# Kernel tuning notes

Hardware: AMD Instinct MI355X
Metric: run time of the kernel (lower is better)

## Reference

```python
import jax, jax.numpy as jnp
import numpy as np

D_MODEL = 1024
NUM_HEADS = 16
WINDOW = 128
DEPTH = D_MODEL // NUM_HEADS


def setup_inputs() -> dict:
    key = jax.random.key(0)
    ks = jax.random.split(key, 9)
    B, S = 2, 2048
    scale = 1.0 / np.sqrt(D_MODEL)
    x = jax.random.normal(ks[0], (B, S, D_MODEL), dtype=jnp.float32)
    Wq = jax.random.normal(ks[1], (D_MODEL, D_MODEL), dtype=jnp.float32) * scale
    Wk = jax.random.normal(ks[2], (D_MODEL, D_MODEL), dtype=jnp.float32) * scale
    Wv = jax.random.normal(ks[3], (D_MODEL, D_MODEL), dtype=jnp.float32) * scale
    Wo = jax.random.normal(ks[4], (D_MODEL, D_MODEL), dtype=jnp.float32) * scale
    bq = jnp.zeros((D_MODEL,), jnp.float32)
    bk = jnp.zeros((D_MODEL,), jnp.float32)
    bv = jnp.zeros((D_MODEL,), jnp.float32)
    bo = jnp.zeros((D_MODEL,), jnp.float32)
    return {"x": x, "Wq": Wq, "bq": bq, "Wk": Wk, "bk": bk,
            "Wv": Wv, "bv": bv, "Wo": Wo, "bo": bo}


def _split_heads(t, B, S):
    # [B,S,D] -> [B,H,S,depth]
    return t.reshape(B, S, NUM_HEADS, DEPTH).transpose(0, 2, 1, 3)


def reference(x, Wq, bq, Wk, bk, Wv, bv, Wo, bo):
    B, S, _ = x.shape
    q = _split_heads(x @ Wq + bq, B, S)
    k = _split_heads(x @ Wk + bk, B, S)
    v = _split_heads(x @ Wv + bv, B, S)
    scores = jnp.einsum('bhqd,bhkd->bhqk', q, k) / jnp.sqrt(jnp.float32(DEPTH))
    idx = jnp.arange(S)
    # mask[i_row=j, i_col=i] per original: |i - j| <= window (symmetric)
    local = jnp.abs(idx[None, :] - idx[:, None]) <= WINDOW  # [S,S]
    scores = jnp.where(local[None, None], scores, jnp.float32(-1e9))
    attn = jax.nn.softmax(scores, axis=-1)
    out = jnp.einsum('bhqk,bhkd->bhqd', attn, v)
    concat = out.transpose(0, 2, 1, 3).reshape(B, S, D_MODEL)
    return concat @ Wo + bo
```

## Files before the change

### kernel.cpp

```cpp
#include <hip/hip_runtime.h>
#include <cstdint>
#include <cstddef>

typedef __attribute__((ext_vector_type(8))) short short8;
typedef __attribute__((ext_vector_type(4))) short short4v;
typedef __attribute__((ext_vector_type(4))) float f32x4;
typedef short8 bf16x8;

typedef __attribute__((address_space(1))) const unsigned GU;
typedef __attribute__((address_space(3))) unsigned LU;

__device__ __forceinline__ short f2bf(float f) {
  unsigned u = __builtin_bit_cast(unsigned, f);
  u += 0x7fffu + ((u >> 16) & 1u);
  return (short)(u >> 16);
}

__global__ __launch_bounds__(256) void k_prep(const float* __restrict__ x,
                                              const float* __restrict__ W0, const float* __restrict__ W1,
                                              const float* __restrict__ W2, const float* __restrict__ W3,
                                              short* __restrict__ xb, short* __restrict__ WT) {
  __shared__ short T[64 * 72];
  int bid = blockIdx.x;
  int tid = threadIdx.x;
  if (bid < 2048) {
    size_t i = ((size_t)bid * 256 + tid) * 8;
    f32x4 a = *(const f32x4*)(x + i);
    f32x4 b = *(const f32x4*)(x + i + 4);
    short8 o;
#pragma unroll
    for (int j = 0; j < 4; ++j) { o[j] = f2bf(a[j]); o[4 + j] = f2bf(b[j]); }
    *(short8*)(xb + i) = o;
    return;
  }
  bid -= 2048;
  int widx = bid >> 8;
  int t = bid & 255;
  int kr = (t >> 4) * 64, nc = (t & 15) * 64;
  const float* W = widx == 0 ? W0 : widx == 1 ? W1 : widx == 2 ? W2 : W3;
  short* out = WT + (size_t)widx * 1048576;
#pragma unroll
  for (int i = 0; i < 4; ++i) {
    int idx = tid + i * 256;
    int k = idx >> 4, n4 = (idx & 15) << 2;
    f32x4 v = *(const f32x4*)(W + (size_t)(kr + k) * 1024 + nc + n4);
#pragma unroll
    for (int j = 0; j < 4; ++j) T[(n4 + j) * 72 + k] = f2bf(v[j]);
  }
  __syncthreads();
#pragma unroll
  for (int i = 0; i < 2; ++i) {
    int idx = tid + i * 256;
    int n = idx >> 3, k8 = (idx & 7) << 3;
    *(short8*)(out + (size_t)(nc + n) * 1024 + kr + k8) = *(const short8*)&T[n * 72 + k8];
  }
}

__global__ __launch_bounds__(256) void k_tv(const short* __restrict__ v, short* __restrict__ vT) {
  __shared__ short T[64 * 72];
  int bid = blockIdx.x;
  int stile = bid & 31, h = (bid >> 5) & 15, b = bid >> 9;
  int s0 = stile * 64;
  int tid = threadIdx.x;
#pragma unroll
  for (int i = 0; i < 2; ++i) {
    int idx = tid + i * 256;
    int s = idx >> 3, d0 = (idx & 7) << 3;
    short8 vec = *(const short8*)(v + ((size_t)b * 2048 + s0 + s) * 1024 + h * 64 + d0);
#pragma unroll
    for (int j = 0; j < 8; ++j) T[(d0 + j) * 72 + s] = vec[j];
  }
  __syncthreads();
#pragma unroll
  for (int i = 0; i < 2; ++i) {
    int idx = tid + i * 256;
    int d = idx >> 3, s8 = (idx & 7) << 3;
    *(short8*)(vT + (((size_t)b * 16 + h) * 64 + d) * 2048 + s0 + s8) = *(const short8*)&T[d * 72 + s8];
  }
}

__global__ __launch_bounds__(512, 1) void k_gemm256(
    const short* __restrict__ A, const short* __restrict__ BT,
    const float* __restrict__ bias0, const float* __restrict__ bias1, const float* __restrict__ bias2,
    short* __restrict__ outb) {
  __shared__ short S[57344];
  const int tid = threadIdx.x;
  const int lane = tid & 63, w = tid >> 6;
  const int g = lane >> 4, qi = lane & 15;
  const int wm = w >> 2, wn = w & 3;
  int bid = blockIdx.x;
  int swz = (bid & 7) * 32 + (bid >> 3);
  const int tm = swz >> 4, tn = swz & 15;
  const int m0 = tm * 256, n0 = tn * 192;
  const size_t K = 1024;
  const short* Ab = A + (size_t)m0 * K;
  const short* Bb = BT + (size_t)n0 * K;

  auto stage64 = [&](int roff, const short* gbase, int kt) {
    int r = tid >> 3;
    int js = ((tid & 7) ^ (r & 7)) << 3;
    __builtin_amdgcn_global_load_lds((GU*)(gbase + (size_t)r * K + kt * 64 + js),
                                     (LU*)(&S[roff + tid * 8]), 16, 0, 0);
  };
  auto lda_a = [&](int bbase, int mf, int kk) -> bf16x8 {
    int row = (mf & 3) * 16 + qi;
    int reg = wm * 2 + (mf >> 2);
    return *(const bf16x8*)&S[bbase + reg * 4096 + row * 64 + (((kk * 4 + g) ^ (row & 7)) << 3)];
  };
  auto lda_b = [&](int bbase, int nf, int kk) -> bf16x8 {
    int c = wn * 48 + nf * 16 + qi;
    int reg = c >> 6, row = c & 63;
    return *(const bf16x8*)&S[bbase + 16384 + reg * 4096 + row * 64 + (((kk * 4 + g) ^ (row & 7)) << 3)];
  };

  f32x4 acc[8][3];
#pragma unroll
  for (int i = 0; i < 8; ++i)
#pragma unroll
    for (int j = 0; j < 3; ++j) acc[i][j] = (f32x4)(0.0f);

#define MFA(mi, ni, av, bv) \
  acc[mi][ni] = __builtin_amdgcn_mfma_f32_16x16x32_bf16(av, bv, acc[mi][ni], 0, 0, 0)
#define MF12(Aa, Bb_, o) \
  MFA((o)+0,0,(Aa)[(o)+0],(Bb_)[0]); MFA((o)+0,1,(Aa)[(o)+0],(Bb_)[1]); MFA((o)+0,2,(Aa)[(o)+0],(Bb_)[2]); \
  MFA((o)+1,0,(Aa)[(o)+1],(Bb_)[0]); MFA((o)+1,1,(Aa)[(o)+1],(Bb_)[1]); MFA((o)+1,2,(Aa)[(o)+1],(Bb_)[2]); \
  MFA((o)+2,0,(Aa)[(o)+2],(Bb_)[0]); MFA((o)+2,1,(Aa)[(o)+2],(Bb_)[1]); MFA((o)+2,2,(Aa)[(o)+2],(Bb_)[2]); \
  MFA((o)+3,0,(Aa)[(o)+3],(Bb_)[0]); MFA((o)+3,1,(Aa)[(o)+3],(Bb_)[1]); MFA((o)+3,2,(Aa)[(o)+3],(Bb_)[2])
#define SB __builtin_amdgcn_sched_barrier(0)
#define PHASE_TAIL(MFMAS) do { \
    SB; \
    __builtin_amdgcn_s_barrier(); \
    asm volatile("s_waitcnt lgkmcnt(0)" ::: "memory"); \
    SB; \
    __builtin_amdgcn_s_setprio(1); \
    MFMAS; \
    __builtin_amdgcn_s_setprio(0); \
    SB; \
    __builtin_amdgcn_s_barrier(); \
  } while (0)

  stage64(0,     Ab,            0);
  stage64(4096,  Ab + 65536,    0);
  stage64(8192,  Ab + 131072,   0);
  stage64(12288, Ab + 196608,   0);
  stage64(16384, Bb,            0);
  stage64(20480, Bb + 65536,    0);
  stage64(24576, Bb + 131072,   0);
  stage64(28672 + 16384, Bb,          1);
  stage64(28672 + 20480, Bb + 65536,  1);
  stage64(28672 + 24576, Bb + 131072, 1);
  asm volatile("s_waitcnt vmcnt(3)" ::: "memory");
  __builtin_amdgcn_s_barrier();

  for (int t = 0; t < 16; ++t) {
    const int b = t & 1, nb = b ^ 1;
    const int bb = b * 28672, nbb = nb * 28672;
    const int t1 = t + 1 < 15 ? t + 1 : 15;
    const int t2 = t + 2 < 15 ? t + 2 : 15;
    bf16x8 aA[8], aB[3], cA[8], cB[3];

#pragma unroll
    for (int mf = 0; mf < 4; ++mf) aA[mf] = lda_a(bb, mf, 0);
#pragma unroll
    for (int nf = 0; nf < 3; ++nf) aB[nf] = lda_b(bb, nf, 0);
    stage64(nbb,        Ab,         t1);
    stage64(nbb + 4096, Ab + 65536, t1);
    PHASE_TAIL(MF12(aA, aB, 0));
#pragma unroll
    for (int mf = 4; mf < 8; ++mf) aA[mf] = lda_a(bb, mf, 0);
#pragma unroll
    for (int nf = 0; nf < 3; ++nf) cB[nf] = lda_b(bb, nf, 1);
    stage64(nbb + 8192,  Ab + 131072, t1);
    stage64(nbb + 12288, Ab + 196608, t1);
    PHASE_TAIL(MF12(aA, aB, 4));
#pragma unroll
    for (int mf = 0; mf < 4; ++mf) cA[mf] = lda_a(bb, mf, 1);
    stage64(bb + 16384, Bb,         t2);
    stage64(bb + 20480, Bb + 65536, t2);
    PHASE_TAIL(MF12(cA, cB, 0));
#pragma unroll
    for (int mf = 4; mf < 8; ++mf) cA[mf] = lda_a(bb, mf, 1);
    stage64(bb + 24576, Bb + 131072, t2);
    asm volatile("s_waitcnt vmcnt(3)" ::: "memory");
    PHASE_TAIL(MF12(cA, cB, 4));
  }
#undef PHASE_TAIL
#undef MF12
#undef MFA
#undef SB

  asm volatile("s_waitcnt vmcnt(0)" ::: "memory");
  __syncthreads();
  float bv[3];
  int seln[3];
#pragma unroll
  for (int nf = 0; nf < 3; ++nf) {
    int colg = n0 + wn * 48 + nf * 16 + qi;
    int sel = colg >> 10;
    const float* bias = sel == 0 ? bias0 : (sel == 1 ? bias1 : bias2);
    bv[nf] = bias[colg & 1023];
    seln[nf] = sel;
    (void)seln;
  }
  short* Ep = S;
#pragma unroll
  for (int p = 0; p < 2; ++p) {
    __syncthreads();
    if (wm == p) {
#pragma unroll
      for (int mf = 0; mf < 8; ++mf)
#pragma unroll
        for (int nf = 0; nf < 3; ++nf)
#pragma unroll
          for (int j = 0; j < 4; ++j)
            Ep[(mf * 16 + g * 4 + j) * 200 + wn * 48 + nf * 16 + qi] =
                f2bf(acc[mf][nf][j] + bv[nf]);
    }
    __syncthreads();
#pragma unroll
    for (int i = 0; i < 6; ++i) {
      int idx = tid + i * 512;
      int r = idx / 24, c8 = (idx % 24) * 8;
      int grow = m0 + p * 128 + r;
      int colg = n0 + c8;
      int sel = colg >> 10;
      *(short8*)&outb[(size_t)sel * 4194304 + (size_t)grow * 1024 + (colg & 1023)] =
          *(const short8*)&Ep[r * 200 + c8];
    }
  }
}

__global__ __launch_bounds__(256, 2) void k_gemmO(
    const short* __restrict__ A, const short* __restrict__ BT,
    const float* __restrict__ bias0, float* __restrict__ outf) {
  __shared__ short Smem[16384];
  const int tid = threadIdx.x;
  const int lane = tid & 63, w = tid >> 6;
  const int g = lane >> 4, qi = lane & 15;
  const int wr = (w >> 1) * 64, wc = (w & 1) * 64;
  const int m0 = blockIdx.y * 128, n0 = blockIdx.x * 128;
  const size_t K = 1024;
  const short* Ab = A + (size_t)m0 * K;
  const short* Bb = BT + (size_t)n0 * K;

  auto stage = [&](int buf, int k0) {
    short* Asb = Smem + buf * 4096;
    short* Bsb = Smem + 8192 + buf * 4096;
#pragma unroll
    for (int i = 0; i < 2; ++i) {
      int cidx = tid + i * 256;
      int r = cidx >> 2;
      int csw = ((cidx & 3) ^ ((r >> 1) & 3)) << 3;
      __builtin_amdgcn_global_load_lds((GU*)(Ab + (size_t)r * K + k0 + csw),
                                       (LU*)(&Asb[cidx * 8]), 16, 0, 0);
      __builtin_amdgcn_global_load_lds((GU*)(Bb + (size_t)r * K + k0 + csw),
                                       (LU*)(&Bsb[cidx * 8]), 16, 0, 0);
    }
  };

  f32x4 acc[4][4];
#pragma unroll
  for (int i = 0; i < 4; ++i)
#pragma unroll
    for (int j = 0; j < 4; ++j) acc[i][j] = (f32x4)(0.0f);

  stage(0, 0);
  __syncthreads();
  for (int kt = 0; kt < 32; ++kt) {
    int cur = kt & 1;
    if (kt < 31) stage(cur ^ 1, (kt + 1) * 32);
    const short* Asb = Smem + cur * 4096;
    const short* Bsb = Smem + 8192 + cur * 4096;
    bf16x8 a[4], b[4];
#pragma unroll
    for (int mf = 0; mf < 4; ++mf) {
      int R = wr + mf * 16 + qi;
      a[mf] = *(const bf16x8*)&Asb[R * 32 + ((g ^ ((R >> 1) & 3)) << 3)];
    }
#pragma unroll
    for (int nf = 0; nf < 4; ++nf) {
      int R = wc + nf * 16 + qi;
      b[nf] = *(const bf16x8*)&Bsb[R * 32 + ((g ^ ((R >> 1) & 3)) << 3)];
    }
#pragma unroll
    for (int mf = 0; mf < 4; ++mf)
#pragma unroll
      for (int nf = 0; nf < 4; ++nf)
        acc[mf][nf] = __builtin_amdgcn_mfma_f32_16x16x32_bf16(a[mf], b[nf], acc[mf][nf], 0, 0, 0);
    __syncthreads();
  }

  float* Ft = (float*)Smem;
  float bv[4];
#pragma unroll
  for (int nf = 0; nf < 4; ++nf) bv[nf] = bias0[n0 + wc + nf * 16 + qi];
#pragma unroll
  for (int mf = 0; mf < 4; ++mf) {
    __syncthreads();
#pragma unroll
    for (int nf = 0; nf < 4; ++nf)
#pragma unroll
      for (int j = 0; j < 4; ++j)
        Ft[((w >> 1) * 16 + g * 4 + j) * 136 + wc + nf * 16 + qi] = acc[mf][nf][j] + bv[nf];
    __syncthreads();
#pragma unroll
    for (int i = 0; i < 4; ++i) {
      int idx = tid + i * 256;
      int r = idx >> 5, c4 = (idx & 31) << 2;
      int row = m0 + ((r >> 4) << 6) + mf * 16 + (r & 15);
      *(f32x4*)&outf[(size_t)row * 1024 + n0 + c4] = *(const f32x4*)&Ft[r * 136 + c4];
    }
  }
}

__global__ __launch_bounds__(256, 2) void k_attn(const short* __restrict__ qg_,
                                                 const short* __restrict__ kg_,
                                                 const short* __restrict__ vT,
                                                 short* __restrict__ outp) {
  __shared__ short Qs[64 * 72];
  __shared__ short Ks[64 * 72];
  __shared__ short Vs[64 * 72];
  __shared__ short Ps[4][16 * 72];
  int bid = blockIdx.x;
  int qt = bid & 31, h = (bid >> 5) & 15, b = bid >> 9;
  int q0 = qt * 64;
  int tid = threadIdx.x, lane = tid & 63, w = tid >> 6;
  int g = lane >> 4, qi = lane & 15;

  const short* qsrc = qg_ + ((size_t)b * 2048 + q0) * 1024 + h * 64;
#pragma unroll
  for (int i = 0; i < 2; ++i) {
    int idx = tid + i * 256;
    int r = idx >> 3, c = (idx & 7) << 3;
    *(short8*)&Qs[r * 72 + c] = *(const short8*)&qsrc[(size_t)r * 1024 + c];
  }

  float m = -1e30f, l = 0.f;
  f32x4 oacc[4];
#pragma unroll
  for (int i = 0; i < 4; ++i) oacc[i] = (f32x4)(0.0f);
  int qglob = q0 + w * 16 + qi;

  for (int cc = 0; cc < 5; ++cc) {
    int kb0 = q0 - 128 + cc * 64;
    if (kb0 < 0 || kb0 >= 2048) continue;
    __syncthreads();
    const short* ksrc = kg_ + ((size_t)b * 2048 + kb0) * 1024 + h * 64;
    const short* vsrc = vT + ((size_t)(b * 16 + h)) * 64 * 2048 + kb0;
#pragma unroll
    for (int i = 0; i < 2; ++i) {
      int idx = tid + i * 256;
      int r = idx >> 3, c = (idx & 7) << 3;
      *(short8*)&Ks[r * 72 + c] = *(const short8*)&ksrc[(size_t)r * 1024 + c];
      *(short8*)&Vs[r * 72 + c] = *(const short8*)&vsrc[(size_t)r * 2048 + c];
    }
    __syncthreads();

    f32x4 st[4];
#pragma unroll
    for (int i = 0; i < 4; ++i) st[i] = (f32x4)(0.0f);
#pragma unroll
    for (int ds = 0; ds < 2; ++ds) {
      bf16x8 qf = *(const bf16x8*)&Qs[(w * 16 + qi) * 72 + ds * 32 + g * 8];
#pragma unroll
      for (int mf = 0; mf < 4; ++mf) {
        bf16x8 kf = *(const bf16x8*)&Ks[(mf * 16 + qi) * 72 + ds * 32 + g * 8];
        st[mf] = __builtin_amdgcn_mfma_f32_16x16x32_bf16(kf, qf, st[mf], 0, 0, 0);
      }
    }

    float pv[16];
    float pm = -1e30f;
#pragma unroll
    for (int mf = 0; mf < 4; ++mf)
#pragma unroll
      for (int j = 0; j < 4; ++j) {
        int kcol = kb0 + mf * 16 + g * 4 + j;
        float s = st[mf][j] * 0.125f;
        int d = kcol - qglob;
        bool valid = (d >= -128) && (d <= 128);
        s = valid ? s : -1e30f;
        pv[mf * 4 + j] = s;
        pm = fmaxf(pm, s);
      }
    pm = fmaxf(pm, __shfl_xor(pm, 16));
    pm = fmaxf(pm, __shfl_xor(pm, 32));
    float mnew = fmaxf(m, pm);
    float scale = __expf(m - mnew);
    float ls = 0.f;
#pragma unroll
    for (int e = 0; e < 16; ++e) {
      float p = pv[e] > -1e29f ? __expf(pv[e] - mnew) : 0.f;
      pv[e] = p;
      ls += p;
    }
    ls += __shfl_xor(ls, 16);
    ls += __shfl_xor(ls, 32);
    l = l * scale + ls;
    m = mnew;
#pragma unroll
    for (int mf = 0; mf < 4; ++mf) oacc[mf] *= scale;

#pragma unroll
    for (int f = 0; f < 4; ++f) {
      short4v pk;
#pragma unroll
      for (int j = 0; j < 4; ++j) pk[j] = f2bf(pv[f * 4 + j]);
      *(short4v*)&Ps[w][qi * 72 + f * 16 + g * 4] = pk;
    }

#pragma unroll
    for (int ks = 0; ks < 2; ++ks) {
      bf16x8 pf = *(const bf16x8*)&Ps[w][qi * 72 + ks * 32 + g * 8];
#pragma unroll
      for (int mf = 0; mf < 4; ++mf) {
        bf16x8 vf = *(const bf16x8*)&Vs[(mf * 16 + qi) * 72 + ks * 32 + g * 8];
        oacc[mf] = __builtin_amdgcn_mfma_f32_16x16x32_bf16(vf, pf, oacc[mf], 0, 0, 0);
      }
    }
  }

  __syncthreads();
  short* Os = Ks;
  float inv = 1.f / l;
#pragma unroll
  for (int mf = 0; mf < 4; ++mf) {
    short4v pk;
#pragma unroll
    for (int j = 0; j < 4; ++j) pk[j] = f2bf(oacc[mf][j] * inv);
    *(short4v*)&Os[(w * 16 + qi) * 72 + mf * 16 + g * 4] = pk;
  }
  __syncthreads();
  short* dst = outp + ((size_t)b * 2048 + q0) * 1024 + h * 64;
  int r = tid >> 2, c16 = (tid & 3) << 4;
  *(short8*)&dst[(size_t)r * 1024 + c16] = *(const short8*)&Os[r * 72 + c16];
  *(short8*)&dst[(size_t)r * 1024 + c16 + 8] = *(const short8*)&Os[r * 72 + c16 + 8];
}

extern "C" void kernel_launch(void* const* d_in, const int* in_sizes, int n_in,
                              void* d_out, int out_size, void* d_ws, size_t ws_size,
                              hipStream_t stream) {
  const float* x  = (const float*)d_in[0];
  const float* Wq = (const float*)d_in[1];
  const float* bq = (const float*)d_in[2];
  const float* Wk = (const float*)d_in[3];
  const float* bk = (const float*)d_in[4];
  const float* Wv = (const float*)d_in[5];
  const float* bv = (const float*)d_in[6];
  const float* Wo = (const float*)d_in[7];
  const float* bo = (const float*)d_in[8];

  short* ws = (short*)d_ws;
  short* xb       = ws;
  short* qkv      = ws + 4194304;
  short* vbuf     = qkv + 2 * 4194304;
  short* vT       = ws;
  short* attn_out = vbuf;
  short* WT       = ws + 4 * 4194304;

  k_prep<<<3072, 256, 0, stream>>>(x, Wq, Wk, Wv, Wo, xb, WT);
  k_gemm256<<<256, 512, 0, stream>>>(xb, WT, bq, bk, bv, qkv);
  k_tv<<<1024, 256, 0, stream>>>(vbuf, vT);
  k_attn<<<1024, 256, 0, stream>>>(qkv, qkv + 4194304, vT, attn_out);
  {
    dim3 grid(8, 32);
    k_gemmO<<<grid, 256, 0, stream>>>(attn_out, WT + 3 * 1048576, bo, (float*)d_out);
  }
}
```

Before: 87.21 us.

## Fuse V transpose into attention kernel and remap QKV GEMM tile order per XCD

Removes the separate k_tv V-transpose kernel. The attention kernel now reads V in its natural [B,S,D] layout and transposes it into shared memory with a rotated column swizzle, which saves one launch and a full global read/write pass of V. The transposed LDS stores are scalar 16-bit writes, which may cause bank conflicts and extra LDS instructions, and V is now re-transposed for each overlapping key tile. The QKV GEMM also changes its block-to-tile mapping so that each XCD covers a contiguous 4x8 block of output tiles, aiming for better L2 reuse.

Measured after the change: 82.20 us. 5.7% less time.

```diff
diff --git a/kernel.cpp b/kernel.cpp
--- a/kernel.cpp
+++ b/kernel.cpp
@@ -56,29 +56,6 @@
   }
 }
 
-__global__ __launch_bounds__(256) void k_tv(const short* __restrict__ v, short* __restrict__ vT) {
-  __shared__ short T[64 * 72];
-  int bid = blockIdx.x;
-  int stile = bid & 31, h = (bid >> 5) & 15, b = bid >> 9;
-  int s0 = stile * 64;
-  int tid = threadIdx.x;
-#pragma unroll
-  for (int i = 0; i < 2; ++i) {
-    int idx = tid + i * 256;
-    int s = idx >> 3, d0 = (idx & 7) << 3;
-    short8 vec = *(const short8*)(v + ((size_t)b * 2048 + s0 + s) * 1024 + h * 64 + d0);
-#pragma unroll
-    for (int j = 0; j < 8; ++j) T[(d0 + j) * 72 + s] = vec[j];
-  }
-  __syncthreads();
-#pragma unroll
-  for (int i = 0; i < 2; ++i) {
-    int idx = tid + i * 256;
-    int d = idx >> 3, s8 = (idx & 7) << 3;
-    *(short8*)(vT + (((size_t)b * 16 + h) * 64 + d) * 2048 + s0 + s8) = *(const short8*)&T[d * 72 + s8];
-  }
-}
-
 __global__ __launch_bounds__(512, 1) void k_gemm256(
     const short* __restrict__ A, const short* __restrict__ BT,
     const float* __restrict__ bias0, const float* __restrict__ bias1, const float* __restrict__ bias2,
@@ -89,8 +66,9 @@
   const int g = lane >> 4, qi = lane & 15;
   const int wm = w >> 2, wn = w & 3;
   int bid = blockIdx.x;
-  int swz = (bid & 7) * 32 + (bid >> 3);
-  const int tm = swz >> 4, tn = swz & 15;
+  int xcd = bid & 7, ii = bid >> 3;
+  const int tm = (xcd >> 1) * 4 + (ii >> 3);
+  const int tn = (xcd & 1) * 8 + (ii & 7);
   const int m0 = tm * 256, n0 = tn * 192;
   const size_t K = 1024;
   const short* Ab = A + (size_t)m0 * K;
@@ -192,15 +170,12 @@
   asm volatile("s_waitcnt vmcnt(0)" ::: "memory");
   __syncthreads();
   float bv[3];
-  int seln[3];
 #pragma unroll
   for (int nf = 0; nf < 3; ++nf) {
     int colg = n0 + wn * 48 + nf * 16 + qi;
     int sel = colg >> 10;
     const float* bias = sel == 0 ? bias0 : (sel == 1 ? bias1 : bias2);
     bv[nf] = bias[colg & 1023];
-    seln[nf] = sel;
-    (void)seln;
   }
   short* Ep = S;
 #pragma unroll
@@ -315,7 +290,7 @@
 
 __global__ __launch_bounds__(256, 2) void k_attn(const short* __restrict__ qg_,
                                                  const short* __restrict__ kg_,
-                                                 const short* __restrict__ vT,
+                                                 const short* __restrict__ vg_,
                                                  short* __restrict__ outp) {
   __shared__ short Qs[64 * 72];
   __shared__ short Ks[64 * 72];
@@ -346,13 +321,18 @@
     if (kb0 < 0 || kb0 >= 2048) continue;
     __syncthreads();
     const short* ksrc = kg_ + ((size_t)b * 2048 + kb0) * 1024 + h * 64;
-    const short* vsrc = vT + ((size_t)(b * 16 + h)) * 64 * 2048 + kb0;
+    const short* vsrc = vg_ + ((size_t)b * 2048 + kb0) * 1024 + h * 64;
 #pragma unroll
     for (int i = 0; i < 2; ++i) {
       int idx = tid + i * 256;
       int r = idx >> 3, c = (idx & 7) << 3;
       *(short8*)&Ks[r * 72 + c] = *(const short8*)&ksrc[(size_t)r * 1024 + c];
-      *(short8*)&Vs[r * 72 + c] = *(const short8*)&vsrc[(size_t)r * 2048 + c];
+      short8 vv = *(const short8*)&vsrc[(size_t)r * 1024 + c];
+#pragma unroll
+      for (int j = 0; j < 8; ++j) {
+        int d = c + j;
+        Vs[d * 72 + ((r + ((d >> 3) << 3)) & 63)] = vv[j];
+      }
     }
     __syncthreads();
 
@@ -414,7 +394,9 @@
       bf16x8 pf = *(const bf16x8*)&Ps[w][qi * 72 + ks * 32 + g * 8];
 #pragma unroll
       for (int mf = 0; mf < 4; ++mf) {
-        bf16x8 vf = *(const bf16x8*)&Vs[(mf * 16 + qi) * 72 + ks * 32 + g * 8];
+        int dd = mf * 16 + qi;
+        int pc = ((ks * 32 + g * 8) + ((dd >> 3) << 3)) & 63;
+        bf16x8 vf = *(const bf16x8*)&Vs[dd * 72 + pc];
         oacc[mf] = __builtin_amdgcn_mfma_f32_16x16x32_bf16(vf, pf, oacc[mf], 0, 0, 0);
       }
     }
@@ -454,14 +436,12 @@
   short* xb       = ws;
   short* qkv      = ws + 4194304;
   short* vbuf     = qkv + 2 * 4194304;
-  short* vT       = ws;
-  short* attn_out = vbuf;
+  short* attn_out = ws;
   short* WT       = ws + 4 * 4194304;
 
   k_prep<<<3072, 256, 0, stream>>>(x, Wq, Wk, Wv, Wo, xb, WT);
   k_gemm256<<<256, 512, 0, stream>>>(xb, WT, bq, bk, bv, qkv);
-  k_tv<<<1024, 256, 0, stream>>>(vbuf, vT);
-  k_attn<<<1024, 256, 0, stream>>>(qkv, qkv + 4194304, vT, attn_out);
+  k_attn<<<1024, 256, 0, stream>>>(qkv, qkv + 4194304, vbuf, attn_out);
   {
     dim3 grid(8, 32);
     k_gemmO<<<grid, 256, 0, stream>>>(attn_out, WT + 3 * 1048576, bo, (float*)d_out);
```
